# Kernel tuning notes

Measured on AMD Instinct MI355X. Metric: run time of the kernel, lower is better.

## Reference

```python
import jax, jax.numpy as jnp
import numpy as np

D = 3            # sde dimension
M_I = 20         # gaussians per axis -> m = M_I**D = 8000
K = 16384        # batch of positions
SIGMA_I = 1.0    # scalar covariance diagonal
NORMALIZED = True


def _grid_means():
    # uniform grid over domain [-3, 3]^D, matching np.mgrid with m_i points per axis
    axes = [np.linspace(-3.0, 3.0, M_I) for _ in range(D)]
    g = np.stack(np.meshgrid(*axes, indexing='ij'), axis=-1).reshape(-1, D)
    return jnp.asarray(g, dtype=jnp.float32)


def setup_inputs() -> dict:
    key = jax.random.key(0)
    kx, kt = jax.random.split(key)
    x = jax.random.normal(kx, (K, D), dtype=jnp.float32)
    means = _grid_means()                      # (m, d)
    theta = jax.random.normal(kt, (means.shape[0],), dtype=jnp.float32)
    return {"x": x, "means": means, "theta": theta}


def reference(x, means, theta):
    # x: (K, d), means: (m, d), theta: (m,)
    sigma = jnp.float32(SIGMA_I)
    diff = x[:, None, :] - means[None, :, :]                  # (K, m, d)
    log_basis = -0.5 * jnp.sum(diff * diff, axis=2) / sigma   # (K, m)
    if NORMALIZED:
        log_basis = log_basis - jnp.float32(np.log(2.0 * np.pi * SIGMA_I) * D / 2.0)
    basis = jnp.exp(log_basis)                                # (K, m)
    # grad basis = -(diff / sigma) * basis[..., None]; weighted sum over m
    out = -jnp.einsum('kmd,km,m->kd', diff, basis, theta) / sigma
    return out
```

## Files before the change

kernel.cpp:

```cpp
#include <hip/hip_runtime.h>


#define NG  20
#define KPB 512
#define KB  64
#define NW  8

__global__ __launch_bounds__(KPB, 2) void gauss_factored_kernel(
    const float* __restrict__ x, const float* __restrict__ means,
    const float* __restrict__ theta, float* __restrict__ out) {
  __shared__ float sred[NW * KB * 3];

  const int tid = threadIdx.x;
  const int lane = tid & 63;
  const int g = __builtin_amdgcn_readfirstlane(tid >> 6);

  const int k = blockIdx.x * KB + lane;
  const float x0 = x[k * 3 + 0];
  const float x1 = x[k * 3 + 1];
  const float x2 = x[k * 3 + 2];

  float Ez[NG], Ezp[NG];
#pragma unroll
  for (int l = 0; l < NG; ++l) {
    const float dz = x2 - means[l * 3 + 2];
    const float e = __expf(-0.5f * dz * dz);
    Ez[l] = e;
    Ezp[l] = -dz * e;
  }

  float o0 = 0.f, o1 = 0.f, o2 = 0.f;
  const int ij0 = g * 50;

#pragma unroll 10
  for (int p = 0; p < 50; ++p) {
    const int ij = ij0 + p;
    const int i = ij / NG, j = ij % NG;
    const float gi = means[i * 1200];
    const float gj = means[j * 60 + 1];
    const float dx = x0 - gi;
    const float dy = x1 - gj;
    const float exy = __expf(-0.5f * fmaf(dx, dx, dy * dy));

    const float* __restrict__ th = theta + ij * NG;
    float aZ0 = 0.f, aZ1 = 0.f, aZp0 = 0.f, aZp1 = 0.f;
#pragma unroll
    for (int l = 0; l < NG; l += 2) {
      const float t0 = th[l], t1 = th[l + 1];
      aZ0  = fmaf(t0, Ez [l],     aZ0);
      aZp0 = fmaf(t0, Ezp[l],     aZp0);
      aZ1  = fmaf(t1, Ez [l + 1], aZ1);
      aZp1 = fmaf(t1, Ezp[l + 1], aZp1);
    }
    const float aZ = aZ0 + aZ1;
    const float aZp = aZp0 + aZp1;
    o0 = fmaf(-dx * exy, aZ,  o0);
    o1 = fmaf(-dy * exy, aZ,  o1);
    o2 = fmaf(      exy, aZp, o2);
  }

  float* sr = &sred[(g * KB + lane) * 3];
  sr[0] = o0; sr[1] = o1; sr[2] = o2;
  __syncthreads();

  if (tid < KB * 3) {
    float s = 0.f;
#pragma unroll
    for (int g2 = 0; g2 < NW; ++g2) s += sred[g2 * (KB * 3) + tid];
    const float Nc = 0.06349363593424097f;
    out[blockIdx.x * (KB * 3) + tid] = s * Nc;
  }
}

extern "C" void kernel_launch(void* const* d_in, const int* in_sizes, int n_in,
                              void* d_out, int out_size, void* d_ws, size_t ws_size,
                              hipStream_t stream) {
  const float* x = (const float*)d_in[0];
  const float* means = (const float*)d_in[1];
  const float* theta = (const float*)d_in[2];
  float* out = (float*)d_out;

  const int K = in_sizes[0] / 3;

  dim3 grid(K / KB);
  gauss_factored_kernel<<<grid, KPB, 0, stream>>>(x, means, theta, out);
}
```

Before: 75.17 us.

## Stage theta and grid coordinates in LDS and double waves per block

Copies the full theta table and the per-axis grid coordinates into shared memory at block start, then reads theta rows as float4 from LDS instead of global memory. Block size doubles to 16 waves so each wave handles fewer (i,j) pairs, and the pair loop is fully unrolled. This aims to remove repeated global/scalar loads and raise per-CU wave count. The cost is a per-block 32KB LDS fill and a barrier, plus higher register pressure from full unrolling at one block per CU.

```diff
diff --git a/kernel.cpp b/kernel.cpp
--- a/kernel.cpp
+++ b/kernel.cpp
@@ -1,19 +1,35 @@
 #include <hip/hip_runtime.h>
 
 
-#define NG  20
-#define KPB 512
-#define KB  64
-#define NW  8
+#define NG    20
+#define NPAIR (NG * NG)
+#define KPB   1024
+#define KB    64
+#define NW    16
+#define PPW   (NPAIR / NW)
 
-__global__ __launch_bounds__(KPB, 2) void gauss_factored_kernel(
+__global__ __launch_bounds__(KPB, 1) void gauss_factored_kernel(
     const float* __restrict__ x, const float* __restrict__ means,
     const float* __restrict__ theta, float* __restrict__ out) {
+  __shared__ float sth[NPAIR * NG];
+  __shared__ float sg[3 * NG];
   __shared__ float sred[NW * KB * 3];
 
   const int tid = threadIdx.x;
   const int lane = tid & 63;
   const int g = __builtin_amdgcn_readfirstlane(tid >> 6);
+
+  {
+    const float4* th4 = (const float4*)theta;
+    float4* s4 = (float4*)sth;
+    for (int idx = tid; idx < NPAIR * NG / 4; idx += KPB) s4[idx] = th4[idx];
+  }
+  if (tid < 3 * NG) {
+    const int axis = tid / NG, p = tid % NG;
+    const int m = (axis == 0) ? p * 400 : (axis == 1) ? p * 20 : p;
+    sg[tid] = means[m * 3 + axis];
+  }
+  __syncthreads();
 
   const int k = blockIdx.x * KB + lane;
   const float x0 = x[k * 3 + 0];
@@ -23,34 +39,36 @@
   float Ez[NG], Ezp[NG];
 #pragma unroll
   for (int l = 0; l < NG; ++l) {
-    const float dz = x2 - means[l * 3 + 2];
+    const float dz = x2 - sg[2 * NG + l];
     const float e = __expf(-0.5f * dz * dz);
     Ez[l] = e;
     Ezp[l] = -dz * e;
   }
 
   float o0 = 0.f, o1 = 0.f, o2 = 0.f;
-  const int ij0 = g * 50;
+  const int p0 = g * PPW;
 
-#pragma unroll 10
-  for (int p = 0; p < 50; ++p) {
-    const int ij = ij0 + p;
+#pragma unroll
+  for (int p = 0; p < PPW; ++p) {
+    const int ij = p0 + p;
     const int i = ij / NG, j = ij % NG;
-    const float gi = means[i * 1200];
-    const float gj = means[j * 60 + 1];
-    const float dx = x0 - gi;
-    const float dy = x1 - gj;
+    const float dx = x0 - sg[i];
+    const float dy = x1 - sg[NG + j];
     const float exy = __expf(-0.5f * fmaf(dx, dx, dy * dy));
 
-    const float* __restrict__ th = theta + ij * NG;
+    const float4* trow = (const float4*)(sth + ij * NG);
     float aZ0 = 0.f, aZ1 = 0.f, aZp0 = 0.f, aZp1 = 0.f;
 #pragma unroll
-    for (int l = 0; l < NG; l += 2) {
-      const float t0 = th[l], t1 = th[l + 1];
-      aZ0  = fmaf(t0, Ez [l],     aZ0);
-      aZp0 = fmaf(t0, Ezp[l],     aZp0);
-      aZ1  = fmaf(t1, Ez [l + 1], aZ1);
-      aZp1 = fmaf(t1, Ezp[l + 1], aZp1);
+    for (int l4 = 0; l4 < 5; ++l4) {
+      const float4 t = trow[l4];
+      aZ0  = fmaf(t.x, Ez [4 * l4 + 0], aZ0);
+      aZp0 = fmaf(t.x, Ezp[4 * l4 + 0], aZp0);
+      aZ1  = fmaf(t.y, Ez [4 * l4 + 1], aZ1);
+      aZp1 = fmaf(t.y, Ezp[4 * l4 + 1], aZp1);
+      aZ0  = fmaf(t.z, Ez [4 * l4 + 2], aZ0);
+      aZp0 = fmaf(t.z, Ezp[4 * l4 + 2], aZp0);
+      aZ1  = fmaf(t.w, Ez [4 * l4 + 3], aZ1);
+      aZp1 = fmaf(t.w, Ezp[4 * l4 + 3], aZp1);
     }
     const float aZ = aZ0 + aZ1;
     const float aZp = aZp0 + aZp1;
```

After: 66.88 us. 1.12x faster.
